# Kernel optimization log

Measured on AMD Instinct MI355X. Metric: run time of the kernel, lower is better.

The kernel has to match this reference:

```python
import jax, jax.numpy as jnp
import numpy as np

N, NFEAT, NHID, OUT, E, P = 50000, 256, 128, 64, 800000, 3
WALK_STEPS, LAMBDA_RW = 13, 0.2


def spmm(row, col, val, x):
    # sparse (N,N) @ dense (N,d) via gather + segment-sum over destination rows
    return jax.ops.segment_sum(val[:, None] * x[col], row, num_segments=N)


def telu(x):
    return x * jnp.tanh(jnp.exp(x))


def setup_inputs() -> dict:
    key = jax.random.key(0)
    ks = jax.random.split(key, 24)
    s = 0.05
    inp = {
        'feature': jax.random.normal(ks[0], (N, NFEAT), jnp.float32),
        'edge_index': jax.random.randint(ks[1], (P, 2, E), 0, N, jnp.int64),
        'edge_val': jax.random.uniform(ks[2], (P, E), jnp.float32) / 16.0,
        'spec_w1': jax.random.normal(ks[3], (P, NFEAT, NHID)) * s,
        'spec_b1': jax.random.normal(ks[4], (P, NHID)) * s,
        'spec_w2': jax.random.normal(ks[5], (P, NHID, OUT)) * s,
        'spec_b2': jax.random.normal(ks[6], (P, OUT)) * s,
        'shared_w1': jax.random.normal(ks[7], (NFEAT, NHID)) * s,
        'shared_b1': jax.random.normal(ks[8], (NHID,)) * s,
        'shared_w2': jax.random.normal(ks[9], (NHID, OUT)) * s,
        'shared_b2': jax.random.normal(ks[10], (OUT,)) * s,
        'weight_b': jax.random.normal(ks[11], (P, 1)) * s,
        'tau': jnp.float32(0.5),
        'mlp_w1': jax.random.normal(ks[12], (OUT * P, NHID)) * s,
        'mlp_b1': jax.random.normal(ks[13], (NHID,)) * s,
        'mlp_w2': jax.random.normal(ks[14], (NHID, OUT)) * s,
        'mlp_b2': jax.random.normal(ks[15], (OUT,)) * s,
        'raw_w1': jax.random.normal(ks[16], (NFEAT, OUT)) * s,
        'raw_b1': jax.random.normal(ks[17], (OUT,)) * s,
        'raw_w2': jax.random.normal(ks[18], (OUT, OUT)) * s,
        'raw_b2': jax.random.normal(ks[19], (OUT,)) * s,
        'proj_w': jax.random.normal(ks[20], (OUT * 4, OUT)) * s,
        'proj_b': jax.random.normal(ks[21], (OUT,)) * s,
    }
    return inp


def reference(feature, edge_index, edge_val, spec_w1, spec_b1, spec_w2, spec_b2,
              shared_w1, shared_b1, shared_w2, shared_b2, weight_b, tau,
              mlp_w1, mlp_b1, mlp_w2, mlp_b2, raw_w1, raw_b1, raw_w2, raw_b2,
              proj_w, proj_b):
    rows = [edge_index[i, 0] for i in range(P)]
    cols = [edge_index[i, 1] for i in range(P)]
    vals = [edge_val[i] for i in range(P)]

    def gc(x, w, b, i):
        return spmm(rows[i], cols[i], vals[i], x @ w) + b

    # path-specific two-layer GCNs (dropout in eval mode = identity)
    specific = []
    for i in range(P):
        h1 = telu(gc(feature, spec_w1[i], spec_b1[i], i))
        specific.append(gc(h1, spec_w2[i], spec_b2[i], i))
    spec_stack = jnp.stack(specific, axis=0)  # (P, N, OUT)

    # shared GCN applied per path
    shared = []
    for i in range(P):
        h1 = telu(gc(feature, shared_w1, shared_b1, i))
        shared.append(gc(h1, shared_w2, shared_b2, i))
    shared_stack = jnp.stack(shared, axis=0)
    H_sh = jnp.mean(shared_stack, axis=0)

    # markov-enhanced path attention
    summaries = []
    for s in specific:
        mean_pool = s.mean(axis=0)
        max_pool = s.max(axis=0)
        p = jax.nn.softmax(s, axis=0)
        entropy = -jnp.sum(p * jnp.log(p + 1e-6), axis=0)
        summaries.append(jnp.concatenate([mean_pool, max_pool, entropy], axis=-1))
    ps = jnp.stack(summaries, axis=0)  # (P, 3*OUT)
    sim = (ps @ ps.T) / (jnp.sqrt(jnp.float32(3 * OUT)) * tau)
    T = jax.nn.softmax(sim, axis=1)
    pi0 = jax.nn.softmax(weight_b.squeeze(-1), axis=0)
    pi = pi0
    for _ in range(WALK_STEPS):
        pi = LAMBDA_RW * pi0 + (1.0 - LAMBDA_RW) * (pi @ T)
    W_tilde = pi[:, None]  # beta dropout is identity in eval mode

    # collaborative MLP on concatenated specific features
    concat_sp = jnp.concatenate(specific, axis=1)  # (N, P*OUT)
    H_col = jax.nn.relu(concat_sp @ mlp_w1 + mlp_b1) @ mlp_w2 + mlp_b2

    # attention-fused specific features
    wprob = jax.nn.softmax(W_tilde, axis=0)[:, 0]  # (P,)
    H_sp_fused = jnp.einsum('pnd,p->nd', spec_stack, wprob)

    # raw path on merged adjacency: final_A = sum_i W_tilde[i] * A_i (applied lazily)
    w = W_tilde[:, 0]

    def merged_spmm(x):
        acc = jnp.zeros((N, x.shape[1]), x.dtype)
        for i in range(P):
            acc = acc + w[i] * spmm(rows[i], cols[i], vals[i], x)
        return acc

    U1 = merged_spmm(feature @ raw_w1) + raw_b1
    U2 = merged_spmm(U1 @ raw_w2) + raw_b2
    H_raw = (U1 + U2) / 2.0

    all_feat = jnp.concatenate([H_sp_fused, H_sh, H_col, H_raw], axis=1)
    out = all_feat @ proj_w + proj_b
    return (out, spec_stack, shared_stack, H_col, H_raw)
```

## Files before the change

### kernel.cpp

```cpp
#include <hip/hip_runtime.h>
#include <hip/hip_bf16.h>
#include <math.h>

#define NN 50000
#define NFEAT 256
#define NHID 128
#define OUTD 64
#define NE 800000
#define NP 3
#define NCH 64
#define RC 782
#define NSB 196
#define NNR (NN + 1)

typedef __hip_bfloat16 bf16;
typedef __attribute__((ext_vector_type(8))) short short8;
typedef __attribute__((ext_vector_type(4))) short short4v;
typedef __attribute__((ext_vector_type(4))) float f32x4;

static inline int cdiv(long a, long b) { return (int)((a + b - 1) / b); }

__device__ __forceinline__ short f2bf(float x) {
    unsigned u = __builtin_bit_cast(unsigned, x);
    unsigned r = (u + 0x7FFFu + ((u >> 16) & 1u)) >> 16;
    return (short)r;
}
__device__ __forceinline__ float bf2f(short b) {
    unsigned u = ((unsigned)(unsigned short)b) << 16;
    return __builtin_bit_cast(float, u);
}

__device__ __forceinline__ void ld8(const float* __restrict__ p, float v[8]) {
    float4 a = *reinterpret_cast<const float4*>(p);
    float4 b = *reinterpret_cast<const float4*>(p + 4);
    v[0] = a.x; v[1] = a.y; v[2] = a.z; v[3] = a.w;
    v[4] = b.x; v[5] = b.y; v[6] = b.z; v[7] = b.w;
}

__device__ __forceinline__ void store4(float* p, const float o[4]) {
    *reinterpret_cast<float4*>(p) = make_float4(o[0], o[1], o[2], o[3]);
}
__device__ __forceinline__ void store4(bf16* p, const float o[4]) {
    short4v u;
    u[0] = f2bf(o[0]); u[1] = f2bf(o[1]); u[2] = f2bf(o[2]); u[3] = f2bf(o[3]);
    *reinterpret_cast<short4v*>(p) = u;
}

__global__ void transpose_split(const float* __restrict__ src, bf16* __restrict__ dh,
                                bf16* __restrict__ dl, int K, int M, long total) {
    long idx = (long)blockIdx.x * blockDim.x + threadIdx.x;
    if (idx >= total) return;
    long pm = idx / K;
    int k = (int)(idx - pm * K);
    long p = pm / M;
    int m = (int)(pm - p * M);
    float v = src[(p * K + k) * M + m];
    short hb = f2bf(v);
    short lb = f2bf(v - bf2f(hb));
    reinterpret_cast<short*>(dh)[idx] = hb;
    reinterpret_cast<short*>(dl)[idx] = lb;
}

template <int K, int M, int MODE, int ACT, typename OT>
__global__ __launch_bounds__(256) void gemm_mfma(
    const float* __restrict__ A, const bf16* __restrict__ Bh, const bf16* __restrict__ Bl,
    const float* __restrict__ bias, OT* __restrict__ out, int nrows,
    const float* __restrict__ wvec, const float* __restrict__ s1,
    const float* __restrict__ s2, const float* __restrict__ s3) {
    constexpr int MC = M / 16;
    __shared__ short AsH[64 * 32];
    __shared__ short AsL[64 * 32];

    int t = threadIdx.x;
    int n0 = blockIdx.x * 64;
    int w = t >> 6;
    int l = t & 63;
    int lr = l & 15, lq = l >> 4;

    float w0 = 0.f, w1 = 0.f, w2 = 0.f;
    if (MODE == 2) { w0 = wvec[3]; w1 = wvec[4]; w2 = wvec[5]; }

    f32x4 acc[MC];
#pragma unroll
    for (int i = 0; i < MC; ++i) {
        f32x4 z = {0.f, 0.f, 0.f, 0.f};
        acc[i] = z;
    }

    int sr = t >> 2, sc = t & 3;
    int gn_s = n0 + sr;
    int wslot = (sc ^ ((sr >> 2) & 3)) << 3;
    short* wpH = &AsH[sr * 32 + wslot];
    short* wpL = &AsL[sr * 32 + wslot];

    int rrow = (w << 4) + lr;
    int roff = rrow * 32 + ((lq ^ ((rrow >> 2) & 3)) << 3);
    const short* rpH = &AsH[roff];
    const short* rpL = &AsL[roff];

    const short* Bhs = reinterpret_cast<const short*>(Bh);
    const short* Bls = reinterpret_cast<const short*>(Bl);

    auto loadA = [&](int k0, float v[8]) {
        if (gn_s >= nrows) {
#pragma unroll
            for (int j = 0; j < 8; ++j) v[j] = 0.f;
            return;
        }
        if (MODE == 0) {
            ld8(A + (long)gn_s * K + k0 + sc * 8, v);
        } else if (MODE == 1) {
            int plane = k0 >> 6;
            int d = (k0 & 63) + sc * 8;
            ld8(A + ((long)plane * NN + gn_s) * OUTD + d, v);
        } else {
            int seg = k0 >> 6;
            int d = (k0 & 63) + sc * 8;
            if (seg == 0) {
                float x0[8], x1[8], x2[8];
                ld8(A + ((long)0 * NN + gn_s) * OUTD + d, x0);
                ld8(A + ((long)1 * NN + gn_s) * OUTD + d, x1);
                ld8(A + ((long)2 * NN + gn_s) * OUTD + d, x2);
#pragma unroll
                for (int j = 0; j < 8; ++j) v[j] = w0 * x0[j] + w1 * x1[j] + w2 * x2[j];
            } else if (seg == 1) {
                float x0[8], x1[8], x2[8];
                ld8(s1 + ((long)0 * NN + gn_s) * OUTD + d, x0);
                ld8(s1 + ((long)1 * NN + gn_s) * OUTD + d, x1);
                ld8(s1 + ((long)2 * NN + gn_s) * OUTD + d, x2);
#pragma unroll
                for (int j = 0; j < 8; ++j) v[j] = (x0[j] + x1[j] + x2[j]) * (1.0f / 3.0f);
            } else if (seg == 2) {
                ld8(s2 + (long)gn_s * OUTD + d, v);
            } else {
                ld8(s3 + (long)gn_s * OUTD + d, v);
            }
        }
    };

    float v[8];
    loadA(0, v);
    for (int k0 = 0; k0 < K; k0 += 32) {
        short8 ah, al;
#pragma unroll
        for (int j = 0; j < 8; ++j) {
            short hb = f2bf(v[j]);
            ah[j] = hb;
            al[j] = f2bf(v[j] - bf2f(hb));
        }
        __syncthreads();
        *reinterpret_cast<short8*>(wpH) = ah;
        *reinterpret_cast<short8*>(wpL) = al;
        __syncthreads();
        if (k0 + 32 < K) loadA(k0 + 32, v);
        short8 fah = *reinterpret_cast<const short8*>(rpH);
        short8 fal = *reinterpret_cast<const short8*>(rpL);
#pragma unroll
        for (int m = 0; m < MC; ++m) {
            long wb = (long)(m * 16 + lr) * K + k0 + (lq << 3);
            short8 bh = *reinterpret_cast<const short8*>(Bhs + wb);
            short8 bl = *reinterpret_cast<const short8*>(Bls + wb);
            acc[m] = __builtin_amdgcn_mfma_f32_16x16x32_bf16(bh, fah, acc[m], 0, 0, 0);
            acc[m] = __builtin_amdgcn_mfma_f32_16x16x32_bf16(bl, fah, acc[m], 0, 0, 0);
            acc[m] = __builtin_amdgcn_mfma_f32_16x16x32_bf16(bh, fal, acc[m], 0, 0, 0);
        }
    }

    int gn = n0 + (w << 4) + lr;
    if (gn < nrows) {
#pragma unroll
        for (int m = 0; m < MC; ++m) {
            int mb = m * 16 + (lq << 2);
            float o[4];
#pragma unroll
            for (int r = 0; r < 4; ++r) {
                o[r] = acc[m][r] + (bias ? bias[mb + r] : 0.f);
                if (ACT == 2) o[r] = fmaxf(o[r], 0.f);
            }
            store4(&out[(long)gn * M + mb], o);
        }
    }
}

__global__ void hist_all(const int* __restrict__ ei, int* __restrict__ cnt) {
    int p = blockIdx.y;
    int e = blockIdx.x * blockDim.x + threadIdx.x;
    if (e >= NE) return;
    int r = ei[((long)p * 2) * NE + e];
    atomicAdd(&cnt[(long)p * NN + r], 1);
}

__global__ void scan_pass1(const int* __restrict__ cnt, int* __restrict__ bsum) {
    int p = blockIdx.y, b = blockIdx.x, t = threadIdx.x;
    int idx = b * 256 + t;
    int v = (idx < NN) ? cnt[(long)p * NN + idx] : 0;
    __shared__ int sh[256];
    sh[t] = v;
    __syncthreads();
    for (int off = 128; off > 0; off >>= 1) {
        if (t < off) sh[t] += sh[t + off];
        __syncthreads();
    }
    if (t == 0) bsum[p * NSB + b] = sh[0];
}

__global__ void scan_pass2(const int* __restrict__ bsum, int* __restrict__ boff) {
    int p = blockIdx.x, t = threadIdx.x;
    int v = (t < NSB) ? bsum[p * NSB + t] : 0;
    __shared__ int sh[256];
    sh[t] = v;
    __syncthreads();
    for (int off = 1; off < 256; off <<= 1) {
        int tmp = (t >= off) ? sh[t - off] : 0;
        __syncthreads();
        sh[t] += tmp;
        __syncthreads();
    }
    if (t < NSB) boff[p * NSB + t] = sh[t] - v;
}

__global__ void scan_pass3(const int* __restrict__ cnt, const int* __restrict__ boff,
                           int* __restrict__ rowptr, int* __restrict__ cursor) {
    int p = blockIdx.y, b = blockIdx.x, t = threadIdx.x;
    int idx = b * 256 + t;
    int v = (idx < NN) ? cnt[(long)p * NN + idx] : 0;
    __shared__ int sh[256];
    sh[t] = v;
    __syncthreads();
    for (int off = 1; off < 256; off <<= 1) {
        int tmp = (t >= off) ? sh[t - off] : 0;
        __syncthreads();
        sh[t] += tmp;
        __syncthreads();
    }
    int rp = boff[p * NSB + b] + sh[t] - v;
    if (idx < NN) {
        rowptr[(long)p * NNR + idx] = rp;
        cursor[(long)p * NN + idx] = rp;
    }
    if (idx == NN - 1) rowptr[(long)p * NNR + NN] = rp + v;
}

__global__ void scatter_all(const int* __restrict__ ei, const float* __restrict__ ev,
                            int* __restrict__ cursor, int* __restrict__ csr_col,
                            float* __restrict__ csr_val) {
    int p = blockIdx.y;
    int e = blockIdx.x * blockDim.x + threadIdx.x;
    if (e >= NE) return;
    int r = ei[((long)p * 2) * NE + e];
    int c = ei[((long)p * 2 + 1) * NE + e];
    float v = ev[(long)p * NE + e];
    int pos = atomicAdd(&cursor[(long)p * NN + r], 1);
    csr_col[(long)p * NE + pos] = c;
    csr_val[(long)p * NE + pos] = v;
}

template <int M, int ACT, int RPB>
__global__ void spmm_dual(const int* __restrict__ rowptr, const int* __restrict__ ccol,
                          const float* __restrict__ cval,
                          const bf16* __restrict__ Ya, const bf16* __restrict__ Yb,
                          const float* __restrict__ biasA, const float* __restrict__ biasB,
                          float* __restrict__ outA, float* __restrict__ outB) {
    constexpr int TPR = M / 2;
    int t = threadIdx.x;
    int n = blockIdx.x * RPB + t / TPR;
    int hs = t % TPR;
    int h = hs * 2;
    if (n >= NN) return;
    int e0 = rowptr[n], e1 = rowptr[n + 1];
    float aAl = biasA[h], aAh = biasA[h + 1];
    float aBl = biasB[h], aBh = biasB[h + 1];
    const unsigned* Ua = reinterpret_cast<const unsigned*>(Ya);
    const unsigned* Ub = reinterpret_cast<const unsigned*>(Yb);
    int e = e0;
    for (; e + 3 < e1; e += 4) {
        int c0 = ccol[e], c1 = ccol[e + 1], c2 = ccol[e + 2], c3 = ccol[e + 3];
        float v0 = cval[e], v1 = cval[e + 1], v2 = cval[e + 2], v3 = cval[e + 3];
        unsigned a0 = Ua[(long)c0 * TPR + hs], a1 = Ua[(long)c1 * TPR + hs];
        unsigned a2 = Ua[(long)c2 * TPR + hs], a3 = Ua[(long)c3 * TPR + hs];
        unsigned b0 = Ub[(long)c0 * TPR + hs], b1 = Ub[(long)c1 * TPR + hs];
        unsigned b2 = Ub[(long)c2 * TPR + hs], b3 = Ub[(long)c3 * TPR + hs];
        aAl += v0 * bf2f((short)a0) + v1 * bf2f((short)a1) + v2 * bf2f((short)a2) + v3 * bf2f((short)a3);
        aAh += v0 * bf2f((short)(a0 >> 16)) + v1 * bf2f((short)(a1 >> 16)) +
               v2 * bf2f((short)(a2 >> 16)) + v3 * bf2f((short)(a3 >> 16));
        aBl += v0 * bf2f((short)b0) + v1 * bf2f((short)b1) + v2 * bf2f((short)b2) + v3 * bf2f((short)b3);
        aBh += v0 * bf2f((short)(b0 >> 16)) + v1 * bf2f((short)(b1 >> 16)) +
               v2 * bf2f((short)(b2 >> 16)) + v3 * bf2f((short)(b3 >> 16));
    }
    for (; e < e1; ++e) {
        int c = ccol[e];
        float v = cval[e];
        unsigned a = Ua[(long)c * TPR + hs];
        unsigned b = Ub[(long)c * TPR + hs];
        aAl += v * bf2f((short)a);
        aAh += v * bf2f((short)(a >> 16));
        aBl += v * bf2f((short)b);
        aBh += v * bf2f((short)(b >> 16));
    }
    if (ACT == 1) {
        aAl = aAl * tanhf(expf(aAl)); aAh = aAh * tanhf(expf(aAh));
        aBl = aBl * tanhf(expf(aBl)); aBh = aBh * tanhf(expf(aBh));
    }
    *reinterpret_cast<float2*>(&outA[(long)n * M + h]) = make_float2(aAl, aAh);
    *reinterpret_cast<float2*>(&outB[(long)n * M + h]) = make_float2(aBl, aBh);
}

__global__ void spmm_merged(const int* __restrict__ rp0, const int* __restrict__ cc0, const float* __restrict__ cv0,
                            const int* __restrict__ rp1, const int* __restrict__ cc1, const float* __restrict__ cv1,
                            const int* __restrict__ rp2, const int* __restrict__ cc2, const float* __restrict__ cv2,
                            const bf16* __restrict__ Y, const float* __restrict__ wvec,
                            const float* __restrict__ bias, float* __restrict__ out) {
    constexpr int TPR = 32;
    int t = threadIdx.x;
    int n = blockIdx.x * 2 + t / TPR;
    int hs = t % TPR;
    int h = hs * 2;
    if (n >= NN) return;
    const int* rps[3] = {rp0, rp1, rp2};
    const int* ccs[3] = {cc0, cc1, cc2};
    const float* cvs[3] = {cv0, cv1, cv2};
    const unsigned* U = reinterpret_cast<const unsigned*>(Y);
    float al = 0.f, ah = 0.f;
#pragma unroll
    for (int p = 0; p < 3; ++p) {
        const int* cc = ccs[p];
        const float* cv = cvs[p];
        int e0 = rps[p][n], e1 = rps[p][n + 1];
        float sl = 0.f, sh = 0.f;
        int e = e0;
        for (; e + 3 < e1; e += 4) {
            int c0 = cc[e], c1 = cc[e + 1], c2 = cc[e + 2], c3 = cc[e + 3];
            float v0 = cv[e], v1 = cv[e + 1], v2 = cv[e + 2], v3 = cv[e + 3];
            unsigned y0 = U[(long)c0 * TPR + hs], y1 = U[(long)c1 * TPR + hs];
            unsigned y2 = U[(long)c2 * TPR + hs], y3 = U[(long)c3 * TPR + hs];
            sl += v0 * bf2f((short)y0) + v1 * bf2f((short)y1) + v2 * bf2f((short)y2) + v3 * bf2f((short)y3);
            sh += v0 * bf2f((short)(y0 >> 16)) + v1 * bf2f((short)(y1 >> 16)) +
                  v2 * bf2f((short)(y2 >> 16)) + v3 * bf2f((short)(y3 >> 16));
        }
        for (; e < e1; ++e) {
            unsigned y = U[(long)cc[e] * TPR + hs];
            float v = cv[e];
            sl += v * bf2f((short)y);
            sh += v * bf2f((short)(y >> 16));
        }
        float wv = wvec[p];
        al += wv * sl;
        ah += wv * sh;
    }
    *reinterpret_cast<float2*>(&out[(long)n * OUTD + h]) =
        make_float2(al + bias[h], ah + bias[h + 1]);
}

__global__ void colsum_passA(const float* __restrict__ spec, float* __restrict__ pmax,
                             float* __restrict__ psum, float* __restrict__ pexp) {
    int p = blockIdx.y, c = blockIdx.x;
    int t = threadIdx.x;
    int d = t & 63, rg = t >> 6;
    const float* base = spec + (long)p * NN * OUTD;
    int r0 = c * RC, r1 = min(r0 + RC, NN);
    float m = -INFINITY, s = 0.f, e = 0.f;
    for (int r = r0 + rg; r < r1; r += 4) {
        float v = base[(long)r * OUTD + d];
        s += v;
        if (v > m) { e = e * __expf(m - v) + 1.0f; m = v; }
        else e += __expf(v - m);
    }
    __shared__ float rm[256], rs[256], re[256];
    rm[t] = m; rs[t] = s; re[t] = e;
    __syncthreads();
    for (int off = 128; off >= 64; off >>= 1) {
        if (t < off) {
            float m2 = fmaxf(rm[t], rm[t + off]);
            re[t] = re[t] * __expf(rm[t] - m2) + re[t + off] * __expf(rm[t + off] - m2);
            rm[t] = m2;
            rs[t] = rs[t] + rs[t + off];
        }
        __syncthreads();
    }
    if (t < 64) {
        long idx = ((long)p * 64 + t) * NCH + c;
        pmax[idx] = rm[t]; psum[idx] = rs[t]; pexp[idx] = re[t];
    }
}

__global__ void colsum_reduceB(const float* __restrict__ pmax, const float* __restrict__ psum,
                               const float* __restrict__ pexp, float* __restrict__ ps,
                               float* __restrict__ zbuf) {
    int b = blockIdx.x;
    int p = b >> 6, d = b & 63;
    int t = threadIdx.x;
    long idx = (long)b * NCH + t;
    float m = pmax[idx], s = psum[idx], e = pexp[idx];
    for (int off = 32; off > 0; off >>= 1) {
        float m2 = fmaxf(m, __shfl_xor(m, off));
        e = e * __expf(m - m2) + __shfl_xor(e, off) * __expf(__shfl_xor(m, off) - m2);
        m = m2;
        s += __shfl_xor(s, off);
    }
    if (t == 0) {
        ps[p * 192 + d] = s / (float)NN;
        ps[p * 192 + 64 + d] = m;
        zbuf[b] = e;
    }
}

__global__ void colsum_passC(const float* __restrict__ spec, const float* __restrict__ ps,
                             const float* __restrict__ zbuf, float* __restrict__ pent) {
    int p = blockIdx.y, c = blockIdx.x;
    int t = threadIdx.x;
    int d = t & 63, rg = t >> 6;
    const float* base = spec + (long)p * NN * OUTD;
    float gm = ps[p * 192 + 64 + d];
    float zinv = 1.0f / zbuf[p * 64 + d];
    int r0 = c * RC, r1 = min(r0 + RC, NN);
    float ent = 0.f;
    for (int r = r0 + rg; r < r1; r += 4) {
        float v = base[(long)r * OUTD + d];
        float pv = __expf(v - gm) * zinv;
        ent -= pv * __logf(pv + 1e-6f);
    }
    __shared__ float rd[256];
    rd[t] = ent;
    __syncthreads();
    for (int off = 128; off >= 64; off >>= 1) {
        if (t < off) rd[t] += rd[t + off];
        __syncthreads();
    }
    if (t < 64) pent[((long)p * 64 + t) * NCH + c] = rd[t];
}

__global__ void colsum_reduceD(const float* __restrict__ pent, float* __restrict__ ps) {
    int b = blockIdx.x;
    int p = b >> 6, d = b & 63;
    int t = threadIdx.x;
    float e = pent[(long)b * NCH + t];
    for (int off = 32; off > 0; off >>= 1) e += __shfl_xor(e, off);
    if (t == 0) ps[p * 192 + 128 + d] = e;
}

__global__ void walk_kernel(const float* __restrict__ ps, const float* __restrict__ weight_b,
                            const float* __restrict__ tau_p, float* __restrict__ wout) {
    if (threadIdx.x != 0 || blockIdx.x != 0) return;
    float sim[3][3];
    float inv = 1.0f / (sqrtf(192.0f) * tau_p[0]);
    for (int i = 0; i < 3; ++i)
        for (int j = 0; j < 3; ++j) {
            float dotv = 0.f;
            for (int k = 0; k < 192; ++k) dotv += ps[i * 192 + k] * ps[j * 192 + k];
            sim[i][j] = dotv * inv;
        }
    float T[3][3];
    for (int i = 0; i < 3; ++i) {
        float m = fmaxf(sim[i][0], fmaxf(sim[i][1], sim[i][2]));
        float e0 = expf(sim[i][0] - m), e1 = expf(sim[i][1] - m), e2 = expf(sim[i][2] - m);
        float s = e0 + e1 + e2;
        T[i][0] = e0 / s; T[i][1] = e1 / s; T[i][2] = e2 / s;
    }
    float b0 = weight_b[0], b1 = weight_b[1], b2 = weight_b[2];
    float m = fmaxf(b0, fmaxf(b1, b2));
    float e0 = expf(b0 - m), e1 = expf(b1 - m), e2 = expf(b2 - m);
    float s = e0 + e1 + e2;
    float pi0[3] = {e0 / s, e1 / s, e2 / s};
    float pi[3] = {pi0[0], pi0[1], pi0[2]};
    for (int it = 0; it < 13; ++it) {
        float n0 = pi[0] * T[0][0] + pi[1] * T[1][0] + pi[2] * T[2][0];
        float n1 = pi[0] * T[0][1] + pi[1] * T[1][1] + pi[2] * T[2][1];
        float n2 = pi[0] * T[0][2] + pi[1] * T[1][2] + pi[2] * T[2][2];
        pi[0] = 0.2f * pi0[0] + 0.8f * n0;
        pi[1] = 0.2f * pi0[1] + 0.8f * n1;
        pi[2] = 0.2f * pi0[2] + 0.8f * n2;
    }
    wout[0] = pi[0]; wout[1] = pi[1]; wout[2] = pi[2];
    float mm = fmaxf(pi[0], fmaxf(pi[1], pi[2]));
    float f0 = expf(pi[0] - mm), f1 = expf(pi[1] - mm), f2 = expf(pi[2] - mm);
    float fs = f0 + f1 + f2;
    wout[3] = f0 / fs; wout[4] = f1 / fs; wout[5] = f2 / fs;
}

__global__ void hraw_final(const float* __restrict__ U1, float* __restrict__ Hraw) {
    long i = (long)blockIdx.x * blockDim.x + threadIdx.x;
    if (i >= (long)NN * OUTD) return;
    Hraw[i] = 0.5f * (U1[i] + Hraw[i]);
}

extern "C" void kernel_launch(void* const* d_in, const int* in_sizes, int n_in,
                              void* d_out, int out_size, void* d_ws, size_t ws_size,
                              hipStream_t stream) {
    const float* feature   = (const float*)d_in[0];
    const int*   edge_index= (const int*)d_in[1];
    const float* edge_val  = (const float*)d_in[2];
    const float* spec_w1   = (const float*)d_in[3];
    const float* spec_b1   = (const float*)d_in[4];
    const float* spec_w2   = (const float*)d_in[5];
    const float* spec_b2   = (const float*)d_in[6];
    const float* shared_w1 = (const float*)d_in[7];
    const float* shared_b1 = (const float*)d_in[8];
    const float* shared_w2 = (const float*)d_in[9];
    const float* shared_b2 = (const float*)d_in[10];
    const float* weight_b  = (const float*)d_in[11];
    const float* tau       = (const float*)d_in[12];
    const float* mlp_w1    = (const float*)d_in[13];
    const float* mlp_b1    = (const float*)d_in[14];
    const float* mlp_w2    = (const float*)d_in[15];
    const float* mlp_b2    = (const float*)d_in[16];
    const float* raw_w1    = (const float*)d_in[17];
    const float* raw_b1    = (const float*)d_in[18];
    const float* raw_w2    = (const float*)d_in[19];
    const float* raw_b2    = (const float*)d_in[20];
    const float* proj_w    = (const float*)d_in[21];
    const float* proj_b    = (const float*)d_in[22];

    float* out        = (float*)d_out;
    float* spec_stack = out + (long)NN * OUTD;
    float* shr_stack  = spec_stack + 3L * NN * OUTD;
    float* Hcol       = out + 7L * NN * OUTD;
    float* Hraw       = out + 8L * NN * OUTD;

    char* wp = (char*)d_ws;
    bf16* XWsh = (bf16*)wp; wp += (long)NN * 128 * sizeof(bf16);
    bf16* XWsp = (bf16*)wp; wp += (long)NN * 128 * sizeof(bf16);
    float* h1sp = (float*)wp; wp += (long)NN * 128 * sizeof(float);
    float* h1sh = (float*)wp; wp += (long)NN * 128 * sizeof(float);
    bf16* Bsp  = (bf16*)wp; wp += (long)NN * OUTD * sizeof(bf16);
    bf16* Bsh  = (bf16*)wp; wp += (long)NN * OUTD * sizeof(bf16);
    float* psBuf = (float*)wp; wp += 1024 * sizeof(float);
    float* wBuf  = (float*)wp; wp += 64 * sizeof(float);
    float* zBuf  = (float*)wp; wp += 256 * sizeof(float);
    float* pMax  = (float*)wp; wp += (long)3 * 64 * NCH * sizeof(float);
    float* pSum  = (float*)wp; wp += (long)3 * 64 * NCH * sizeof(float);
    float* pExp  = (float*)wp; wp += (long)3 * 64 * NCH * sizeof(float);
    float* pEnt  = (float*)wp; wp += (long)3 * 64 * NCH * sizeof(float);
    int*   csr_col_all = (int*)wp;   wp += (long)NP * NE * sizeof(int);
    float* csr_val_all = (float*)wp; wp += (long)NP * NE * sizeof(float);
    int*   rowptr_all  = (int*)wp;   wp += (long)NP * NNR * sizeof(int) + 64;
    int* cnt    = (int*)wp; wp += (long)NP * NN * sizeof(int);
    int* cursor = (int*)wp; wp += (long)NP * NN * sizeof(int);
    int* bsum   = (int*)wp; wp += (long)NP * NSB * sizeof(int);
    int* boff   = (int*)wp; wp += (long)NP * NSB * sizeof(int);
    bf16* w1sp_h = (bf16*)wp; wp += 3L * 256 * 128 * sizeof(bf16);
    bf16* w1sp_l = (bf16*)wp; wp += 3L * 256 * 128 * sizeof(bf16);
    bf16* w1sh_h = (bf16*)wp; wp += 256L * 128 * sizeof(bf16);
    bf16* w1sh_l = (bf16*)wp; wp += 256L * 128 * sizeof(bf16);
    bf16* w2sp_h = (bf16*)wp; wp += 3L * 128 * 64 * sizeof(bf16);
    bf16* w2sp_l = (bf16*)wp; wp += 3L * 128 * 64 * sizeof(bf16);
    bf16* w2sh_h = (bf16*)wp; wp += 128L * 64 * sizeof(bf16);
    bf16* w2sh_l = (bf16*)wp; wp += 128L * 64 * sizeof(bf16);
    bf16* mlp1_h = (bf16*)wp; wp += 192L * 128 * sizeof(bf16);
    bf16* mlp1_l = (bf16*)wp; wp += 192L * 128 * sizeof(bf16);
    bf16* mlp2_h = (bf16*)wp; wp += 128L * 64 * sizeof(bf16);
    bf16* mlp2_l = (bf16*)wp; wp += 128L * 64 * sizeof(bf16);
    bf16* raw1_h = (bf16*)wp; wp += 256L * 64 * sizeof(bf16);
    bf16* raw1_l = (bf16*)wp; wp += 256L * 64 * sizeof(bf16);
    bf16* raw2_h = (bf16*)wp; wp += 64L * 64 * sizeof(bf16);
    bf16* raw2_l = (bf16*)wp; wp += 64L * 64 * sizeof(bf16);
    bf16* proj_h = (bf16*)wp; wp += 256L * 64 * sizeof(bf16);
    bf16* proj_l = (bf16*)wp; wp += 256L * 64 * sizeof(bf16);

    int* rowptr[NP]; int* csr_col[NP]; float* csr_val[NP];
    for (int p = 0; p < NP; ++p) {
        rowptr[p]  = rowptr_all + (long)p * NNR;
        csr_col[p] = csr_col_all + (long)p * NE;
        csr_val[p] = csr_val_all + (long)p * NE;
    }

    const int TB = 256;
    int g_rows = cdiv(NN, 64);

    transpose_split<<<cdiv(3L * 256 * 128, TB), TB, 0, stream>>>(spec_w1, w1sp_h, w1sp_l, 256, 128, 3L * 256 * 128);
    transpose_split<<<cdiv(256L * 128, TB), TB, 0, stream>>>(shared_w1, w1sh_h, w1sh_l, 256, 128, 256L * 128);
    transpose_split<<<cdiv(3L * 128 * 64, TB), TB, 0, stream>>>(spec_w2, w2sp_h, w2sp_l, 128, 64, 3L * 128 * 64);
    transpose_split<<<cdiv(128L * 64, TB), TB, 0, stream>>>(shared_w2, w2sh_h, w2sh_l, 128, 64, 128L * 64);
    transpose_split<<<cdiv(192L * 128, TB), TB, 0, stream>>>(mlp_w1, mlp1_h, mlp1_l, 192, 128, 192L * 128);
    transpose_split<<<cdiv(128L * 64, TB), TB, 0, stream>>>(mlp_w2, mlp2_h, mlp2_l, 128, 64, 128L * 64);
    transpose_split<<<cdiv(256L * 64, TB), TB, 0, stream>>>(raw_w1, raw1_h, raw1_l, 256, 64, 256L * 64);
    transpose_split<<<cdiv(64L * 64, TB), TB, 0, stream>>>(raw_w2, raw2_h, raw2_l, 64, 64, 64L * 64);
    transpose_split<<<cdiv(256L * 64, TB), TB, 0, stream>>>(proj_w, proj_h, proj_l, 256, 64, 256L * 64);

    hipMemsetAsync(cnt, 0, (long)NP * NN * sizeof(int), stream);
    {
        dim3 gE(cdiv(NE, TB), NP);
        hist_all<<<gE, TB, 0, stream>>>(edge_index, cnt);
        dim3 gS(NSB, NP);
        scan_pass1<<<gS, 256, 0, stream>>>(cnt, bsum);
        scan_pass2<<<NP, 256, 0, stream>>>(bsum, boff);
        scan_pass3<<<gS, 256, 0, stream>>>(cnt, boff, rowptr_all, cursor);
        scatter_all<<<gE, TB, 0, stream>>>(edge_index, edge_val, cursor, csr_col_all, csr_val_all);
    }

    gemm_mfma<256, 128, 0, 0, bf16><<<g_rows, 256, 0, stream>>>(
        feature, w1sh_h, w1sh_l, nullptr, XWsh, NN, nullptr, nullptr, nullptr, nullptr);

    for (int p = 0; p < NP; ++p) {
        gemm_mfma<256, 128, 0, 0, bf16><<<g_rows, 256, 0, stream>>>(
            feature, w1sp_h + (long)p * 256 * 128, w1sp_l + (long)p * 256 * 128,
            nullptr, XWsp, NN, nullptr, nullptr, nullptr, nullptr);
        spmm_dual<128, 1, 1><<<NN, 64, 0, stream>>>(rowptr[p], csr_col[p], csr_val[p],
                                                    XWsp, XWsh,
                                                    spec_b1 + (long)p * 128, shared_b1,
                                                    h1sp, h1sh);
        gemm_mfma<128, 64, 0, 0, bf16><<<g_rows, 256, 0, stream>>>(
            h1sp, w2sp_h + (long)p * 128 * 64, w2sp_l + (long)p * 128 * 64,
            nullptr, Bsp, NN, nullptr, nullptr, nullptr, nullptr);
        gemm_mfma<128, 64, 0, 0, bf16><<<g_rows, 256, 0, stream>>>(
            h1sh, w2sh_h, w2sh_l, nullptr, Bsh, NN, nullptr, nullptr, nullptr, nullptr);
        spmm_dual<64, 0, 2><<<cdiv(NN, 2), 64, 0, stream>>>(rowptr[p], csr_col[p], csr_val[p],
                                                            Bsp, Bsh,
                                                            spec_b2 + (long)p * 64, shared_b2,
                                                            spec_stack + (long)p * NN * OUTD,
                                                            shr_stack + (long)p * NN * OUTD);
    }

    {
        dim3 gA(NCH, 3);
        colsum_passA<<<gA, 256, 0, stream>>>(spec_stack, pMax, pSum, pExp);
        colsum_reduceB<<<192, 64, 0, stream>>>(pMax, pSum, pExp, psBuf, zBuf);
        colsum_passC<<<gA, 256, 0, stream>>>(spec_stack, psBuf, zBuf, pEnt);
        colsum_reduceD<<<192, 64, 0, stream>>>(pEnt, psBuf);
    }
    walk_kernel<<<1, 64, 0, stream>>>(psBuf, weight_b, tau, wBuf);

    gemm_mfma<192, 128, 1, 2, float><<<g_rows, 256, 0, stream>>>(
        spec_stack, mlp1_h, mlp1_l, mlp_b1, h1sp, NN, nullptr, nullptr, nullptr, nullptr);
    gemm_mfma<128, 64, 0, 0, float><<<g_rows, 256, 0, stream>>>(
        h1sp, mlp2_h, mlp2_l, mlp_b2, Hcol, NN, nullptr, nullptr, nullptr, nullptr);

    float* U1 = h1sh;
    gemm_mfma<256, 64, 0, 0, bf16><<<g_rows, 256, 0, stream>>>(
        feature, raw1_h, raw1_l, nullptr, Bsp, NN, nullptr, nullptr, nullptr, nullptr);
    spmm_merged<<<cdiv(NN, 2), 64, 0, stream>>>(rowptr[0], csr_col[0], csr_val[0],
                                                rowptr[1], csr_col[1], csr_val[1],
                                                rowptr[2], csr_col[2], csr_val[2],
                                                Bsp, wBuf, raw_b1, U1);
    gemm_mfma<64, 64, 0, 0, bf16><<<g_rows, 256, 0, stream>>>(
        U1, raw2_h, raw2_l, nullptr, Bsh, NN, nullptr, nullptr, nullptr, nullptr);
    spmm_merged<<<cdiv(NN, 2), 64, 0, stream>>>(rowptr[0], csr_col[0], csr_val[0],
                                                rowptr[1], csr_col[1], csr_val[1],
                                                rowptr[2], csr_col[2], csr_val[2],
                                                Bsh, wBuf, raw_b2, Hraw);
    hraw_final<<<cdiv((long)NN * OUTD, TB), TB, 0, stream>>>(U1, Hraw);

    gemm_mfma<256, 64, 2, 0, float><<<g_rows, 256, 0, stream>>>(
        spec_stack, proj_h, proj_l, proj_b, out, NN, wBuf, shr_stack, Hcol, Hraw);
}
```

Measured before the change: 1.575 ms.

## Build CSR via row-bucketed two-phase scatter with interleaved col/val pairs

Replaces the global per-row atomic scatter with a two-phase scheme. Edges are first appended into 256 row buckets, then each block scatters its bucket into CSR using shared-memory row cursors. Column and value are stored together as int2 so the SpMM kernels read one 8-byte record per edge instead of two separate arrays. TeLU now uses fast __expf-based tanh, and the workspace buffers are reordered. Risks: bucket capacity BCAP=4096 must hold about 3136 expected edges per bucket, and it overflows on skewed inputs; one extra pass over the edges is added.

```diff
diff --git a/kernel.cpp b/kernel.cpp
--- a/kernel.cpp
+++ b/kernel.cpp
@@ -12,11 +12,15 @@
 #define RC 782
 #define NSB 196
 #define NNR (NN + 1)
+#define NBUK 256
+#define BROWS 196
+#define BCAP 4096
 
 typedef __hip_bfloat16 bf16;
 typedef __attribute__((ext_vector_type(8))) short short8;
 typedef __attribute__((ext_vector_type(4))) short short4v;
 typedef __attribute__((ext_vector_type(4))) float f32x4;
+typedef unsigned long long u64;
 
 static inline int cdiv(long a, long b) { return (int)((a + b - 1) / b); }
 
@@ -28,6 +32,12 @@
 __device__ __forceinline__ float bf2f(short b) {
     unsigned u = ((unsigned)(unsigned short)b) << 16;
     return __builtin_bit_cast(float, u);
+}
+
+__device__ __forceinline__ float telu_f(float x) {
+    float e = __expf(x);
+    float t = __expf(-2.0f * e);
+    return x * (1.0f - t) / (1.0f + t);
 }
 
 __device__ __forceinline__ void ld8(const float* __restrict__ p, float v[8]) {
@@ -220,7 +230,7 @@
 }
 
 __global__ void scan_pass3(const int* __restrict__ cnt, const int* __restrict__ boff,
-                           int* __restrict__ rowptr, int* __restrict__ cursor) {
+                           int* __restrict__ rowptr) {
     int p = blockIdx.y, b = blockIdx.x, t = threadIdx.x;
     int idx = b * 256 + t;
     int v = (idx < NN) ? cnt[(long)p * NN + idx] : 0;
@@ -234,30 +244,50 @@
         __syncthreads();
     }
     int rp = boff[p * NSB + b] + sh[t] - v;
-    if (idx < NN) {
-        rowptr[(long)p * NNR + idx] = rp;
-        cursor[(long)p * NN + idx] = rp;
-    }
+    if (idx < NN) rowptr[(long)p * NNR + idx] = rp;
     if (idx == NN - 1) rowptr[(long)p * NNR + NN] = rp + v;
 }
 
-__global__ void scatter_all(const int* __restrict__ ei, const float* __restrict__ ev,
-                            int* __restrict__ cursor, int* __restrict__ csr_col,
-                            float* __restrict__ csr_val) {
+__global__ void bucket_append(const int* __restrict__ ei, int* __restrict__ bcnt,
+                              int* __restrict__ bbuf) {
     int p = blockIdx.y;
     int e = blockIdx.x * blockDim.x + threadIdx.x;
     if (e >= NE) return;
     int r = ei[((long)p * 2) * NE + e];
-    int c = ei[((long)p * 2 + 1) * NE + e];
-    float v = ev[(long)p * NE + e];
-    int pos = atomicAdd(&cursor[(long)p * NN + r], 1);
-    csr_col[(long)p * NE + pos] = c;
-    csr_val[(long)p * NE + pos] = v;
+    int b = r / BROWS;
+    int pos = atomicAdd(&bcnt[p * NBUK + b], 1);
+    bbuf[((long)p * NBUK + b) * BCAP + pos] = e;
+}
+
+__global__ __launch_bounds__(256) void bucket_scatter(
+    const int* __restrict__ ei, const float* __restrict__ ev,
+    const int* __restrict__ bcnt, const int* __restrict__ bbuf,
+    const int* __restrict__ rowptr, int2* __restrict__ csr) {
+    int b = blockIdx.x, p = blockIdx.y;
+    int t = threadIdx.x;
+    int row0 = b * BROWS;
+    int nrows = min(BROWS, NN - row0);
+    __shared__ int cur[BROWS];
+    for (int i = t; i < nrows; i += 256) cur[i] = rowptr[(long)p * NNR + row0 + i];
+    __syncthreads();
+    int cntb = bcnt[p * NBUK + b];
+    const int* buf = bbuf + ((long)p * NBUK + b) * BCAP;
+    const int* rs = ei + ((long)p * 2) * NE;
+    const int* cs = rs + NE;
+    const float* vs = ev + (long)p * NE;
+    int2* csrp = csr + (long)p * NE;
+    for (int i = t; i < cntb; i += 256) {
+        int e = buf[i];
+        int r = rs[e];
+        int c = cs[e];
+        float v = vs[e];
+        int pos = atomicAdd(&cur[r - row0], 1);
+        csrp[pos] = make_int2(c, __float_as_int(v));
+    }
 }
 
 template <int M, int ACT, int RPB>
-__global__ void spmm_dual(const int* __restrict__ rowptr, const int* __restrict__ ccol,
-                          const float* __restrict__ cval,
+__global__ void spmm_dual(const int* __restrict__ rowptr, const int2* __restrict__ csr,
                           const bf16* __restrict__ Ya, const bf16* __restrict__ Yb,
                           const float* __restrict__ biasA, const float* __restrict__ biasB,
                           float* __restrict__ outA, float* __restrict__ outB) {
@@ -274,12 +304,13 @@
     const unsigned* Ub = reinterpret_cast<const unsigned*>(Yb);
     int e = e0;
     for (; e + 3 < e1; e += 4) {
-        int c0 = ccol[e], c1 = ccol[e + 1], c2 = ccol[e + 2], c3 = ccol[e + 3];
-        float v0 = cval[e], v1 = cval[e + 1], v2 = cval[e + 2], v3 = cval[e + 3];
-        unsigned a0 = Ua[(long)c0 * TPR + hs], a1 = Ua[(long)c1 * TPR + hs];
-        unsigned a2 = Ua[(long)c2 * TPR + hs], a3 = Ua[(long)c3 * TPR + hs];
-        unsigned b0 = Ub[(long)c0 * TPR + hs], b1 = Ub[(long)c1 * TPR + hs];
-        unsigned b2 = Ub[(long)c2 * TPR + hs], b3 = Ub[(long)c3 * TPR + hs];
+        int2 p0 = csr[e], p1 = csr[e + 1], p2 = csr[e + 2], p3 = csr[e + 3];
+        unsigned a0 = Ua[(long)p0.x * TPR + hs], a1 = Ua[(long)p1.x * TPR + hs];
+        unsigned a2 = Ua[(long)p2.x * TPR + hs], a3 = Ua[(long)p3.x * TPR + hs];
+        unsigned b0 = Ub[(long)p0.x * TPR + hs], b1 = Ub[(long)p1.x * TPR + hs];
+        unsigned b2 = Ub[(long)p2.x * TPR + hs], b3 = Ub[(long)p3.x * TPR + hs];
+        float v0 = __int_as_float(p0.y), v1 = __int_as_float(p1.y);
+        float v2 = __int_as_float(p2.y), v3 = __int_as_float(p3.y);
         aAl += v0 * bf2f((short)a0) + v1 * bf2f((short)a1) + v2 * bf2f((short)a2) + v3 * bf2f((short)a3);
         aAh += v0 * bf2f((short)(a0 >> 16)) + v1 * bf2f((short)(a1 >> 16)) +
                v2 * bf2f((short)(a2 >> 16)) + v3 * bf2f((short)(a3 >> 16));
@@ -288,26 +319,26 @@
                v2 * bf2f((short)(b2 >> 16)) + v3 * bf2f((short)(b3 >> 16));
     }
     for (; e < e1; ++e) {
-        int c = ccol[e];
-        float v = cval[e];
-        unsigned a = Ua[(long)c * TPR + hs];
-        unsigned b = Ub[(long)c * TPR + hs];
+        int2 pe = csr[e];
+        float v = __int_as_float(pe.y);
+        unsigned a = Ua[(long)pe.x * TPR + hs];
+        unsigned b = Ub[(long)pe.x * TPR + hs];
         aAl += v * bf2f((short)a);
         aAh += v * bf2f((short)(a >> 16));
         aBl += v * bf2f((short)b);
         aBh += v * bf2f((short)(b >> 16));
     }
     if (ACT == 1) {
-        aAl = aAl * tanhf(expf(aAl)); aAh = aAh * tanhf(expf(aAh));
-        aBl = aBl * tanhf(expf(aBl)); aBh = aBh * tanhf(expf(aBh));
+        aAl = telu_f(aAl); aAh = telu_f(aAh);
+        aBl = telu_f(aBl); aBh = telu_f(aBh);
     }
     *reinterpret_cast<float2*>(&outA[(long)n * M + h]) = make_float2(aAl, aAh);
     *reinterpret_cast<float2*>(&outB[(long)n * M + h]) = make_float2(aBl, aBh);
 }
 
-__global__ void spmm_merged(const int* __restrict__ rp0, const int* __restrict__ cc0, const float* __restrict__ cv0,
-                            const int* __restrict__ rp1, const int* __restrict__ cc1, const float* __restrict__ cv1,
-                            const int* __restrict__ rp2, const int* __restrict__ cc2, const float* __restrict__ cv2,
+__global__ void spmm_merged(const int* __restrict__ rp0, const int2* __restrict__ cs0,
+                            const int* __restrict__ rp1, const int2* __restrict__ cs1,
+                            const int* __restrict__ rp2, const int2* __restrict__ cs2,
                             const bf16* __restrict__ Y, const float* __restrict__ wvec,
                             const float* __restrict__ bias, float* __restrict__ out) {
     constexpr int TPR = 32;
@@ -317,29 +348,29 @@
     int h = hs * 2;
     if (n >= NN) return;
     const int* rps[3] = {rp0, rp1, rp2};
-    const int* ccs[3] = {cc0, cc1, cc2};
-    const float* cvs[3] = {cv0, cv1, cv2};
+    const int2* css[3] = {cs0, cs1, cs2};
     const unsigned* U = reinterpret_cast<const unsigned*>(Y);
     float al = 0.f, ah = 0.f;
 #pragma unroll
     for (int p = 0; p < 3; ++p) {
-        const int* cc = ccs[p];
-        const float* cv = cvs[p];
+        const int2* cs = css[p];
         int e0 = rps[p][n], e1 = rps[p][n + 1];
         float sl = 0.f, sh = 0.f;
         int e = e0;
         for (; e + 3 < e1; e += 4) {
-            int c0 = cc[e], c1 = cc[e + 1], c2 = cc[e + 2], c3 = cc[e + 3];
-            float v0 = cv[e], v1 = cv[e + 1], v2 = cv[e + 2], v3 = cv[e + 3];
-            unsigned y0 = U[(long)c0 * TPR + hs], y1 = U[(long)c1 * TPR + hs];
-            unsigned y2 = U[(long)c2 * TPR + hs], y3 = U[(long)c3 * TPR + hs];
+            int2 p0 = cs[e], p1 = cs[e + 1], p2 = cs[e + 2], p3 = cs[e + 3];
+            unsigned y0 = U[(long)p0.x * TPR + hs], y1 = U[(long)p1.x * TPR + hs];
+            unsigned y2 = U[(long)p2.x * TPR + hs], y3 = U[(long)p3.x * TPR + hs];
+            float v0 = __int_as_float(p0.y), v1 = __int_as_float(p1.y);
+            float v2 = __int_as_float(p2.y), v3 = __int_as_float(p3.y);
             sl += v0 * bf2f((short)y0) + v1 * bf2f((short)y1) + v2 * bf2f((short)y2) + v3 * bf2f((short)y3);
             sh += v0 * bf2f((short)(y0 >> 16)) + v1 * bf2f((short)(y1 >> 16)) +
                   v2 * bf2f((short)(y2 >> 16)) + v3 * bf2f((short)(y3 >> 16));
         }
         for (; e < e1; ++e) {
-            unsigned y = U[(long)cc[e] * TPR + hs];
-            float v = cv[e];
+            int2 pe = cs[e];
+            unsigned y = U[(long)pe.x * TPR + hs];
+            float v = __int_as_float(pe.y);
             sl += v * bf2f((short)y);
             sh += v * bf2f((short)(y >> 16));
         }
@@ -517,12 +548,12 @@
     float* Hraw       = out + 8L * NN * OUTD;
 
     char* wp = (char*)d_ws;
+    bf16* XWsp = (bf16*)wp; wp += (long)NN * 128 * sizeof(bf16);
     bf16* XWsh = (bf16*)wp; wp += (long)NN * 128 * sizeof(bf16);
-    bf16* XWsp = (bf16*)wp; wp += (long)NN * 128 * sizeof(bf16);
+    bf16* Bsp  = (bf16*)wp; wp += (long)NN * OUTD * sizeof(bf16);
+    bf16* Bsh  = (bf16*)wp; wp += (long)NN * OUTD * sizeof(bf16);
     float* h1sp = (float*)wp; wp += (long)NN * 128 * sizeof(float);
     float* h1sh = (float*)wp; wp += (long)NN * 128 * sizeof(float);
-    bf16* Bsp  = (bf16*)wp; wp += (long)NN * OUTD * sizeof(bf16);
-    bf16* Bsh  = (bf16*)wp; wp += (long)NN * OUTD * sizeof(bf16);
     float* psBuf = (float*)wp; wp += 1024 * sizeof(float);
     float* wBuf  = (float*)wp; wp += 64 * sizeof(float);
     float* zBuf  = (float*)wp; wp += 256 * sizeof(float);
@@ -530,13 +561,13 @@
     float* pSum  = (float*)wp; wp += (long)3 * 64 * NCH * sizeof(float);
     float* pExp  = (float*)wp; wp += (long)3 * 64 * NCH * sizeof(float);
     float* pEnt  = (float*)wp; wp += (long)3 * 64 * NCH * sizeof(float);
-    int*   csr_col_all = (int*)wp;   wp += (long)NP * NE * sizeof(int);
-    float* csr_val_all = (float*)wp; wp += (long)NP * NE * sizeof(float);
-    int*   rowptr_all  = (int*)wp;   wp += (long)NP * NNR * sizeof(int) + 64;
+    int2* csr_all = (int2*)wp;  wp += (long)NP * NE * sizeof(int2);
+    int*  rowptr_all = (int*)wp; wp += (long)NP * NNR * sizeof(int) + 64;
     int* cnt    = (int*)wp; wp += (long)NP * NN * sizeof(int);
-    int* cursor = (int*)wp; wp += (long)NP * NN * sizeof(int);
     int* bsum   = (int*)wp; wp += (long)NP * NSB * sizeof(int);
     int* boff   = (int*)wp; wp += (long)NP * NSB * sizeof(int);
+    int* bcnt   = (int*)wp; wp += (long)NP * NBUK * sizeof(int);
+    int* bbuf   = (int*)wp; wp += (long)NP * NBUK * BCAP * sizeof(int);
     bf16* w1sp_h = (bf16*)wp; wp += 3L * 256 * 128 * sizeof(bf16);
     bf16* w1sp_l = (bf16*)wp; wp += 3L * 256 * 128 * sizeof(bf16);
     bf16* w1sh_h = (bf16*)wp; wp += 256L * 128 * sizeof(bf16);
@@ -556,11 +587,10 @@
     bf16* proj_h = (bf16*)wp; wp += 256L * 64 * sizeof(bf16);
     bf16* proj_l = (bf16*)wp; wp += 256L * 64 * sizeof(bf16);
 
-    int* rowptr[NP]; int* csr_col[NP]; float* csr_val[NP];
+    int* rowptr[NP]; int2* csr[NP];
     for (int p = 0; p < NP; ++p) {
-        rowptr[p]  = rowptr_all + (long)p * NNR;
-        csr_col[p] = csr_col_all + (long)p * NE;
-        csr_val[p] = csr_val_all + (long)p * NE;
+        rowptr[p] = rowptr_all + (long)p * NNR;
+        csr[p]    = csr_all + (long)p * NE;
     }
 
     const int TB = 256;
@@ -577,14 +607,18 @@
     transpose_split<<<cdiv(256L * 64, TB), TB, 0, stream>>>(proj_w, proj_h, proj_l, 256, 64, 256L * 64);
 
     hipMemsetAsync(cnt, 0, (long)NP * NN * sizeof(int), stream);
+    hipMemsetAsync(bcnt, 0, (long)NP * NBUK * sizeof(int), stream);
     {
         dim3 gE(cdiv(NE, TB), NP);
         hist_all<<<gE, TB, 0, stream>>>(edge_index, cnt);
+        bucket_append<<<gE, TB, 0, stream>>>(edge_index, bcnt, bbuf);
         dim3 gS(NSB, NP);
         scan_pass1<<<gS, 256, 0, stream>>>(cnt, bsum);
         scan_pass2<<<NP, 256, 0, stream>>>(bsum, boff);
-        scan_pass3<<<gS, 256, 0, stream>>>(cnt, boff, rowptr_all, cursor);
-        scatter_all<<<gE, TB, 0, stream>>>(edge_index, edge_val, cursor, csr_col_all, csr_val_all);
+        scan_pass3<<<gS, 256, 0, stream>>>(cnt, boff, rowptr_all);
+        dim3 gB(NBUK, NP);
+        bucket_scatter<<<gB, 256, 0, stream>>>(edge_index, edge_val, bcnt, bbuf,
+                                               rowptr_all, csr_all);
     }
 
     gemm_mfma<256, 128, 0, 0, bf16><<<g_rows, 256, 0, stream>>>(
@@ -594,8 +628,7 @@
         gemm_mfma<256, 128, 0, 0, bf16><<<g_rows, 256, 0, stream>>>(
             feature, w1sp_h + (long)p * 256 * 128, w1sp_l + (long)p * 256 * 128,
             nullptr, XWsp, NN, nullptr, nullptr, nullptr, nullptr);
-        spmm_dual<128, 1, 1><<<NN, 64, 0, stream>>>(rowptr[p], csr_col[p], csr_val[p],
-                                                    XWsp, XWsh,
+        spmm_dual<128, 1, 1><<<NN, 64, 0, stream>>>(rowptr[p], csr[p], XWsp, XWsh,
                                                     spec_b1 + (long)p * 128, shared_b1,
                                                     h1sp, h1sh);
         gemm_mfma<128, 64, 0, 0, bf16><<<g_rows, 256, 0, stream>>>(
@@ -603,8 +636,7 @@
             nullptr, Bsp, NN, nullptr, nullptr, nullptr, nullptr);
         gemm_mfma<128, 64, 0, 0, bf16><<<g_rows, 256, 0, stream>>>(
             h1sh, w2sh_h, w2sh_l, nullptr, Bsh, NN, nullptr, nullptr, nullptr, nullptr);
-        spmm_dual<64, 0, 2><<<cdiv(NN, 2), 64, 0, stream>>>(rowptr[p], csr_col[p], csr_val[p],
-                                                            Bsp, Bsh,
+        spmm_dual<64, 0, 2><<<cdiv(NN, 2), 64, 0, stream>>>(rowptr[p], csr[p], Bsp, Bsh,
                                                             spec_b2 + (long)p * 64, shared_b2,
                                                             spec_stack + (long)p * NN * OUTD,
                                                             shr_stack + (long)p * NN * OUTD);
@@ -627,15 +659,15 @@
     float* U1 = h1sh;
     gemm_mfma<256, 64, 0, 0, bf16><<<g_rows, 256, 0, stream>>>(
         feature, raw1_h, raw1_l, nullptr, Bsp, NN, nullptr, nullptr, nullptr, nullptr);
-    spmm_merged<<<cdiv(NN, 2), 64, 0, stream>>>(rowptr[0], csr_col[0], csr_val[0],
-                                                rowptr[1], csr_col[1], csr_val[1],
-                                                rowptr[2], csr_col[2], csr_val[2],
+    spmm_merged<<<cdiv(NN, 2), 64, 0, stream>>>(rowptr[0], csr[0],
+                                                rowptr[1], csr[1],
+                                                rowptr[2], csr[2],
                                                 Bsp, wBuf, raw_b1, U1);
     gemm_mfma<64, 64, 0, 0, bf16><<<g_rows, 256, 0, stream>>>(
         U1, raw2_h, raw2_l, nullptr, Bsh, NN, nullptr, nullptr, nullptr, nullptr);
-    spmm_merged<<<cdiv(NN, 2), 64, 0, stream>>>(rowptr[0], csr_col[0], csr_val[0],
-                                                rowptr[1], csr_col[1], csr_val[1],
-                                                rowptr[2], csr_col[2], csr_val[2],
+    spmm_merged<<<cdiv(NN, 2), 64, 0, stream>>>(rowptr[0], csr[0],
+                                                rowptr[1], csr[1],
+                                                rowptr[2], csr[2],
                                                 Bsh, wBuf, raw_b2, Hraw);
     hraw_final<<<cdiv((long)NN * OUTD, TB), TB, 0, stream>>>(U1, Hraw);
 
```

Measured after the change: 2.366 ms. +50.2%, slower.
